# Kernel optimization log

Hardware: AMD Instinct MI355X
Metric: run time of the kernel (lower is better)

Reference implementation:

```python
import jax, jax.numpy as jnp
import numpy as np

B, N, DIM, H = 2, 192, 512, 8
Dh = DIM // H
SCALE = Dh ** -0.5


def setup_inputs() -> dict:
    key = jax.random.key(0)
    ks = jax.random.split(key, 13)
    s = 0.02

    def w(k):
        return jax.random.normal(k, (DIM, DIM), dtype=jnp.float32) * s

    def b(k):
        return jax.random.normal(k, (DIM,), dtype=jnp.float32) * s

    return {
        "queries": jax.random.normal(ks[0], (B, N, DIM), dtype=jnp.float32),
        "keys": jax.random.normal(ks[1], (B, N, DIM), dtype=jnp.float32),
        "values": jax.random.normal(ks[2], (B, N, DIM), dtype=jnp.float32),
        "Wq": w(ks[3]), "bq": b(ks[4]),
        "Wk": w(ks[5]), "bk": b(ks[6]),
        "Wl": w(ks[7]), "bl": b(ks[8]),
        "Wv": w(ks[9]), "bv": b(ks[10]),
        "Wp": w(ks[11]), "bp": b(ks[12]),
    }


def _split_heads(x):
    # [B, N, DIM] -> [B, H, N, Dh]
    return x.reshape(B, N, H, Dh).transpose(0, 2, 1, 3)


def reference(queries, keys, values, Wq, bq, Wk, bk, Wl, bl, Wv, bv, Wp, bp):
    q = _split_heads(queries @ Wq.T + bq) * SCALE
    k = _split_heads(keys @ Wk.T + bk)
    l = _split_heads(keys @ Wl.T + bl)
    v = _split_heads(values @ Wv.T + bv)
    # third-order scores: [B, H, N, N, N]
    attn = jnp.einsum('bhid,bhjd,bhkd->bhijk', q, k, l)
    # softmax over flattened (j, k) axis (valid_lens=None path)
    attn = jax.nn.softmax(attn.reshape(B, H, N, N * N), axis=-1).reshape(B, H, N, N, N)
    # contraction with v_map[b,h,j,k,d] = v[b,h,j,d]*v[b,h,k,d], fused (same math)
    x = jnp.einsum('bhijk,bhjd,bhkd->bhid', attn, v, v)
    x = x.transpose(0, 2, 1, 3).reshape(B, N, DIM)  # merge heads
    return x @ Wp.T + bp
```

## Files before the change

### kernel.cpp

```cpp
#include <hip/hip_runtime.h>

#define B_ 2
#define N_ 192
#define DIM_ 512
#define H_ 8
#define DH_ 64
#define PROJ_ELEMS (B_*H_*N_*DH_)
#define W_ELEMS (DIM_*DIM_)
#define A_ELEMS (B_*N_*DIM_)

typedef __bf16 bf16_t;
typedef __bf16 bf16x4 __attribute__((ext_vector_type(4)));
typedef __bf16 bf16x8 __attribute__((ext_vector_type(8)));
typedef float  f32x16 __attribute__((ext_vector_type(16)));

__device__ __forceinline__ f32x16 mfma32(bf16x8 a, bf16x8 b, f32x16 c) {
    return __builtin_amdgcn_mfma_f32_32x32x16_bf16(a, b, c, 0, 0, 0);
}

union U4 { unsigned int u[4]; bf16x8 v; };

__device__ __forceinline__ unsigned int pack_bf16(float a, float b) {
    unsigned short ua = __builtin_bit_cast(unsigned short, (bf16_t)a);
    unsigned short ub = __builtin_bit_cast(unsigned short, (bf16_t)b);
    return (unsigned int)ua | ((unsigned int)ub << 16);
}
__device__ __forceinline__ float bfbits(unsigned short u) {
    return (float)__builtin_bit_cast(bf16_t, u);
}

struct CArgs {
    const float* src[8];
    bf16_t* dst[8];
    int n[8];
};
__global__ __launch_bounds__(256) void cvt_kernel(CArgs a) {
    const int s = blockIdx.y;
    const int i = (blockIdx.x * 256 + threadIdx.x) * 4;
    if (i < a.n[s]) {
        float4 v = *(const float4*)(a.src[s] + i);
        bf16x4 o;
        o[0] = (bf16_t)v.x; o[1] = (bf16_t)v.y; o[2] = (bf16_t)v.z; o[3] = (bf16_t)v.w;
        *(bf16x4*)(a.dst[s] + i) = o;
    }
}

struct GArgs {
    const bf16_t* A[4];
    const bf16_t* Bm[4];
    const float* bias[4];
    float scale[4];
};

template<int MODE>
__global__ __launch_bounds__(256) void gemm64_kernel(GArgs g, void* outp) {
    const int mat = blockIdx.y;
    const bf16_t* __restrict__ A  = g.A[mat];
    const bf16_t* __restrict__ Bm = g.Bm[mat];

    const int rt = blockIdx.x >> 3, ct = blockIdx.x & 7;
    const int r0 = rt * 64, c0 = ct * 64;
    const int tid = threadIdx.x, wid = tid >> 6, lane = tid & 63;
    const int lo = lane & 31, hi = lane >> 5;
    const int wr = wid >> 1, wc = wid & 1;

    __shared__ __attribute__((aligned(16))) bf16_t As[64 * 64];
    __shared__ __attribute__((aligned(16))) bf16_t Bs[64 * 64];

    f32x16 acc = {};
    for (int k0 = 0; k0 < DIM_; k0 += 64) {
        #pragma unroll
        for (int cch = 0; cch < 2; ++cch) {
            const int d = wid * 2048 + cch * 1024 + lane * 16;
            const int r = d >> 7;
            const int off = (d ^ ((r & 7) << 4)) & 127;
            const char* srcA = (const char*)A + (size_t)(r0 + r) * (DIM_ * 2) + k0 * 2 + off;
            const char* srcB = (const char*)Bm + (size_t)(c0 + r) * (DIM_ * 2) + k0 * 2 + off;
            __builtin_amdgcn_global_load_lds(
                (const __attribute__((address_space(1))) void*)srcA,
                (__attribute__((address_space(3))) void*)((char*)As + wid * 2048 + cch * 1024),
                16, 0, 0);
            __builtin_amdgcn_global_load_lds(
                (const __attribute__((address_space(1))) void*)srcB,
                (__attribute__((address_space(3))) void*)((char*)Bs + wid * 2048 + cch * 1024),
                16, 0, 0);
        }
        __syncthreads();
        const int rowA = wr * 32 + lo, rowB = wc * 32 + lo;
        #pragma unroll
        for (int s = 0; s < 4; ++s) {
            const int ka = (rowA * 128 + s * 32 + hi * 16) ^ ((rowA & 7) << 4);
            const int kb = (rowB * 128 + s * 32 + hi * 16) ^ ((rowB & 7) << 4);
            bf16x8 af = *(const bf16x8*)((const char*)As + ka);
            bf16x8 bf = *(const bf16x8*)((const char*)Bs + kb);
            acc = mfma32(af, bf, acc);
        }
        __syncthreads();
    }

    const int c = c0 + wc * 32 + lo;
    const float bv = g.bias[mat][c];
    if (MODE == 0) {
        const float sc = g.scale[mat];
        const int h = c >> 6, dd = c & 63;
        bf16_t* out = (bf16_t*)outp + (size_t)mat * PROJ_ELEMS;
        #pragma unroll
        for (int r = 0; r < 16; ++r) {
            int row = r0 + wr * 32 + (r & 3) + 8 * (r >> 2) + 4 * hi;
            int bb = (row >= N_) ? 1 : 0;
            int n = row - bb * N_;
            out[(((size_t)(bb * H_ + h)) * N_ + n) * DH_ + dd] = (bf16_t)((acc[r] + bv) * sc);
        }
    } else {
        float* out = (float*)outp;
        #pragma unroll
        for (int r = 0; r < 16; ++r) {
            int row = r0 + wr * 32 + (r & 3) + 8 * (r >> 2) + 4 * hi;
            out[(size_t)row * DIM_ + c] = acc[r] + bv;
        }
    }
}

__global__ __launch_bounds__(256, 3) void attn_kernel(
    const bf16_t* __restrict__ Qg, const bf16_t* __restrict__ Kg,
    const bf16_t* __restrict__ Lg, const bf16_t* __restrict__ Vg,
    bf16_t* __restrict__ Xout)
{
    __shared__ __attribute__((aligned(16))) bf16_t Llds[192 * 72];
    __shared__ __attribute__((aligned(16))) bf16_t VTlds[64 * 200];

    const int bh = blockIdx.y;
    const int tid = threadIdx.x, wid = tid >> 6, lane = tid & 63;
    const int lo = lane & 31, hi = lane >> 5;
    const size_t base = (size_t)bh * (N_ * DH_);

    for (int idx = tid; idx < 1536; idx += 256) {
        int row = idx >> 3, ch = idx & 7;
        *(uint4*)&Llds[row * 72 + ch * 8] = *(const uint4*)(Lg + base + row * 64 + ch * 8);
    }
    for (int idx = tid; idx < 1536; idx += 256) {
        int dc = idx / 192, j = idx - dc * 192;
        bf16x8 v = *(const bf16x8*)(Vg + base + (size_t)j * 64 + dc * 8);
        #pragma unroll
        for (int u = 0; u < 8; ++u)
            VTlds[(dc * 8 + u) * 200 + j] = v[u];
    }
    __syncthreads();

    const int i = blockIdx.x * 4 + wid;
    const bf16_t* qp = Qg + base + (size_t)i * 64;
    bf16x8 qb[4];
    #pragma unroll
    for (int s = 0; s < 4; ++s) qb[s] = *(const bf16x8*)(qp + s * 16 + hi * 8);

    float xacc0 = 0.f, xacc1 = 0.f;
    float Zp[4] = {0.f, 0.f, 0.f, 0.f};

    for (int jb = 0; jb < 6; ++jb) {
        bf16x8 bq[4];
        const bf16_t* kp = Kg + base + (size_t)(jb * 32 + lo) * 64;
        #pragma unroll
        for (int s = 0; s < 4; ++s) {
            bf16x8 kv = *(const bf16x8*)(kp + s * 16 + hi * 8);
            bf16x8 t;
            #pragma unroll
            for (int u = 0; u < 8; ++u) t[u] = (bf16_t)((float)kv[u] * (float)qb[s][u]);
            bq[s] = t;
        }

        f32x16 Tc0 = {}, Tc1 = {};
        #pragma unroll
        for (int kh = 0; kh < 2; ++kh) {
            f32x16 Sc[3];
            #pragma unroll
            for (int kt = 0; kt < 3; ++kt) {
                f32x16 a = {};
                #pragma unroll
                for (int s = 0; s < 4; ++s) {
                    bf16x8 lf = *(const bf16x8*)&Llds[(kh * 96 + kt * 32 + lo) * 72 + s * 16 + hi * 8];
                    a = mfma32(lf, bq[s], a);
                }
                Sc[kt] = a;
            }
            #pragma unroll
            for (int kt = 0; kt < 3; ++kt) {
                float e[16];
                #pragma unroll
                for (int r = 0; r < 16; ++r) {
                    e[r] = __builtin_amdgcn_exp2f(Sc[kt][r]);
                    Zp[r & 3] += e[r];
                }
                #pragma unroll
                for (int sg = 0; sg < 2; ++sg) {
                    unsigned int x0 = pack_bf16(e[8*sg+0], e[8*sg+1]);
                    unsigned int x1 = pack_bf16(e[8*sg+2], e[8*sg+3]);
                    unsigned int y0 = pack_bf16(e[8*sg+4], e[8*sg+5]);
                    unsigned int y1 = pack_bf16(e[8*sg+6], e[8*sg+7]);
                    asm volatile("v_permlane32_swap_b32 %0, %1\n\t"
                                 "v_permlane32_swap_b32 %2, %3"
                                 : "+v"(x0), "+v"(y0), "+v"(x1), "+v"(y1));
                    U4 uf; uf.u[0] = x0; uf.u[1] = x1; uf.u[2] = y0; uf.u[3] = y1;
                    const int tg = kh * 6 + kt * 2 + sg;
                    bf16x8 vf0 = *(const bf16x8*)&VTlds[(0 * 32 + lo) * 200 + tg * 16 + hi * 8];
                    Tc0 = mfma32(uf.v, vf0, Tc0);
                    bf16x8 vf1 = *(const bf16x8*)&VTlds[(1 * 32 + lo) * 200 + tg * 16 + hi * 8];
                    Tc1 = mfma32(uf.v, vf1, Tc1);
                }
            }
        }
        #pragma unroll
        for (int m = 0; m < 4; ++m) {
            const int jj = jb * 32 + m * 8 + 4 * hi;
            ushort4 v0 = *(const ushort4*)&VTlds[(0 * 32 + lo) * 200 + jj];
            ushort4 v1 = *(const ushort4*)&VTlds[(1 * 32 + lo) * 200 + jj];
            xacc0 += Tc0[m*4+0]*bfbits(v0.x) + Tc0[m*4+1]*bfbits(v0.y)
                   + Tc0[m*4+2]*bfbits(v0.z) + Tc0[m*4+3]*bfbits(v0.w);
            xacc1 += Tc1[m*4+0]*bfbits(v1.x) + Tc1[m*4+1]*bfbits(v1.y)
                   + Tc1[m*4+2]*bfbits(v1.z) + Tc1[m*4+3]*bfbits(v1.w);
        }
    }

    float Z = (Zp[0] + Zp[1]) + (Zp[2] + Zp[3]);
    Z += __shfl_xor(Z, 1);
    Z += __shfl_xor(Z, 2);
    Z += __shfl_xor(Z, 4);
    Z += __shfl_xor(Z, 8);
    Z += __shfl_xor(Z, 16);
    Z += __shfl_xor(Z, 32);
    xacc0 += __shfl_xor(xacc0, 32);
    xacc1 += __shfl_xor(xacc1, 32);
    const float invZ = 1.0f / Z;

    if (hi == 0) {
        const int b = bh >> 3, h = bh & 7;
        bf16_t* op = Xout + ((size_t)(b * N_ + i) * DIM_) + h * 64;
        op[lo]      = (bf16_t)(xacc0 * invZ);
        op[32 + lo] = (bf16_t)(xacc1 * invZ);
    }
}

extern "C" void kernel_launch(void* const* d_in, const int* in_sizes, int n_in,
                              void* d_out, int out_size, void* d_ws, size_t ws_size,
                              hipStream_t stream) {
    (void)in_sizes; (void)n_in; (void)out_size; (void)ws_size;
    const float* queries = (const float*)d_in[0];
    const float* keys    = (const float*)d_in[1];
    const float* values  = (const float*)d_in[2];
    const float* Wq = (const float*)d_in[3];
    const float* bq = (const float*)d_in[4];
    const float* Wk = (const float*)d_in[5];
    const float* bk = (const float*)d_in[6];
    const float* Wl = (const float*)d_in[7];
    const float* bl = (const float*)d_in[8];
    const float* Wv = (const float*)d_in[9];
    const float* bv = (const float*)d_in[10];
    const float* Wp = (const float*)d_in[11];
    const float* bp = (const float*)d_in[12];

    bf16_t* Abf = (bf16_t*)d_ws;
    bf16_t* Wbf = Abf + 3 * (size_t)A_ELEMS;
    bf16_t* Pw  = Wbf + 5 * (size_t)W_ELEMS;
    bf16_t* Xw  = Pw  + 4 * (size_t)PROJ_ELEMS;

    CArgs ca;
    ca.src[0] = queries; ca.dst[0] = Abf;               ca.n[0] = A_ELEMS;
    ca.src[1] = keys;    ca.dst[1] = Abf + A_ELEMS;     ca.n[1] = A_ELEMS;
    ca.src[2] = values;  ca.dst[2] = Abf + 2*A_ELEMS;   ca.n[2] = A_ELEMS;
    ca.src[3] = Wq;      ca.dst[3] = Wbf;               ca.n[3] = W_ELEMS;
    ca.src[4] = Wk;      ca.dst[4] = Wbf + W_ELEMS;     ca.n[4] = W_ELEMS;
    ca.src[5] = Wl;      ca.dst[5] = Wbf + 2*W_ELEMS;   ca.n[5] = W_ELEMS;
    ca.src[6] = Wv;      ca.dst[6] = Wbf + 3*W_ELEMS;   ca.n[6] = W_ELEMS;
    ca.src[7] = Wp;      ca.dst[7] = Wbf + 4*W_ELEMS;   ca.n[7] = W_ELEMS;
    cvt_kernel<<<dim3(256, 8), 256, 0, stream>>>(ca);

    GArgs pa;
    pa.A[0] = Abf;             pa.Bm[0] = Wbf;             pa.bias[0] = bq; pa.scale[0] = 0.125f * 1.44269504f;
    pa.A[1] = Abf + A_ELEMS;   pa.Bm[1] = Wbf + W_ELEMS;   pa.bias[1] = bk; pa.scale[1] = 1.0f;
    pa.A[2] = Abf + A_ELEMS;   pa.Bm[2] = Wbf + 2*W_ELEMS; pa.bias[2] = bl; pa.scale[2] = 1.0f;
    pa.A[3] = Abf + 2*A_ELEMS; pa.Bm[3] = Wbf + 3*W_ELEMS; pa.bias[3] = bv; pa.scale[3] = 1.0f;
    gemm64_kernel<0><<<dim3(48, 4), 256, 0, stream>>>(pa, (void*)Pw);

    attn_kernel<<<dim3(48, 16), 256, 0, stream>>>(
        Pw, Pw + PROJ_ELEMS, Pw + 2 * (size_t)PROJ_ELEMS, Pw + 3 * (size_t)PROJ_ELEMS, Xw);

    GArgs fa;
    fa.A[0] = Xw; fa.Bm[0] = Wbf + 4*W_ELEMS; fa.bias[0] = bp; fa.scale[0] = 1.0f;
    fa.A[1] = fa.A[0]; fa.Bm[1] = fa.Bm[0]; fa.bias[1] = fa.bias[0]; fa.scale[1] = 1.0f;
    fa.A[2] = fa.A[0]; fa.Bm[2] = fa.Bm[0]; fa.bias[2] = fa.bias[0]; fa.scale[2] = 1.0f;
    fa.A[3] = fa.A[0]; fa.Bm[3] = fa.Bm[0]; fa.bias[3] = fa.bias[0]; fa.scale[3] = 1.0f;
    gemm64_kernel<1><<<dim3(48, 1), 256, 0, stream>>>(fa, d_out);
}
```

Before: 137.1 us.

## Split k-range across wave pairs and read L from global instead of LDS

Each query row is now handled by two waves, each covering half of the k dimension, and the partial outputs and normalizers are combined through shared memory. The grid doubles to 96x16 blocks. The L tile is no longer staged in LDS; each wave reads its L fragments directly from global memory (cached in L1/L2). Together with the smaller LDS footprint this allows raising launch bounds to 4 blocks per CU, aiming for more parallelism and occupancy. In exchange it repeats global L loads in every jb iteration and adds a block-level reduction with an extra barrier.

```diff
diff --git a/kernel.cpp b/kernel.cpp
--- a/kernel.cpp
+++ b/kernel.cpp
@@ -121,23 +121,21 @@
     }
 }
 
-__global__ __launch_bounds__(256, 3) void attn_kernel(
+__global__ __launch_bounds__(256, 4) void attn_kernel(
     const bf16_t* __restrict__ Qg, const bf16_t* __restrict__ Kg,
     const bf16_t* __restrict__ Lg, const bf16_t* __restrict__ Vg,
     bf16_t* __restrict__ Xout)
 {
-    __shared__ __attribute__((aligned(16))) bf16_t Llds[192 * 72];
     __shared__ __attribute__((aligned(16))) bf16_t VTlds[64 * 200];
-
-    const int bh = blockIdx.y;
+    __shared__ float Xbuf[2][2][64];
+    __shared__ float Zbuf[2][2];
+
     const int tid = threadIdx.x, wid = tid >> 6, lane = tid & 63;
     const int lo = lane & 31, hi = lane >> 5;
+    const int ip = wid >> 1, half = wid & 1;
+    const int bh = blockIdx.y;
     const size_t base = (size_t)bh * (N_ * DH_);
 
-    for (int idx = tid; idx < 1536; idx += 256) {
-        int row = idx >> 3, ch = idx & 7;
-        *(uint4*)&Llds[row * 72 + ch * 8] = *(const uint4*)(Lg + base + row * 64 + ch * 8);
-    }
     for (int idx = tid; idx < 1536; idx += 256) {
         int dc = idx / 192, j = idx - dc * 192;
         bf16x8 v = *(const bf16x8*)(Vg + base + (size_t)j * 64 + dc * 8);
@@ -147,7 +145,7 @@
     }
     __syncthreads();
 
-    const int i = blockIdx.x * 4 + wid;
+    const int i = blockIdx.x * 2 + ip;
     const bf16_t* qp = Qg + base + (size_t)i * 64;
     bf16x8 qb[4];
     #pragma unroll
@@ -168,44 +166,43 @@
             bq[s] = t;
         }
 
+        f32x16 Sc[3];
+        #pragma unroll
+        for (int kt = 0; kt < 3; ++kt) {
+            f32x16 a = {};
+            const bf16_t* lrow = Lg + base + (size_t)(half * 96 + kt * 32 + lo) * 64;
+            #pragma unroll
+            for (int s = 0; s < 4; ++s) {
+                bf16x8 lf = *(const bf16x8*)(lrow + s * 16 + hi * 8);
+                a = mfma32(lf, bq[s], a);
+            }
+            Sc[kt] = a;
+        }
+
         f32x16 Tc0 = {}, Tc1 = {};
         #pragma unroll
-        for (int kh = 0; kh < 2; ++kh) {
-            f32x16 Sc[3];
-            #pragma unroll
-            for (int kt = 0; kt < 3; ++kt) {
-                f32x16 a = {};
-                #pragma unroll
-                for (int s = 0; s < 4; ++s) {
-                    bf16x8 lf = *(const bf16x8*)&Llds[(kh * 96 + kt * 32 + lo) * 72 + s * 16 + hi * 8];
-                    a = mfma32(lf, bq[s], a);
-                }
-                Sc[kt] = a;
+        for (int kt = 0; kt < 3; ++kt) {
+            float e[16];
+            #pragma unroll
+            for (int r = 0; r < 16; ++r) {
+                e[r] = __builtin_amdgcn_exp2f(Sc[kt][r]);
+                Zp[r & 3] += e[r];
             }
             #pragma unroll
-            for (int kt = 0; kt < 3; ++kt) {
-                float e[16];
-                #pragma unroll
-                for (int r = 0; r < 16; ++r) {
-                    e[r] = __builtin_amdgcn_exp2f(Sc[kt][r]);
-                    Zp[r & 3] += e[r];
-                }
-                #pragma unroll
-                for (int sg = 0; sg < 2; ++sg) {
-                    unsigned int x0 = pack_bf16(e[8*sg+0], e[8*sg+1]);
-                    unsigned int x1 = pack_bf16(e[8*sg+2], e[8*sg+3]);
-                    unsigned int y0 = pack_bf16(e[8*sg+4], e[8*sg+5]);
-                    unsigned int y1 = pack_bf16(e[8*sg+6], e[8*sg+7]);
-                    asm volatile("v_permlane32_swap_b32 %0, %1\n\t"
-                                 "v_permlane32_swap_b32 %2, %3"
-                                 : "+v"(x0), "+v"(y0), "+v"(x1), "+v"(y1));
-                    U4 uf; uf.u[0] = x0; uf.u[1] = x1; uf.u[2] = y0; uf.u[3] = y1;
-                    const int tg = kh * 6 + kt * 2 + sg;
-                    bf16x8 vf0 = *(const bf16x8*)&VTlds[(0 * 32 + lo) * 200 + tg * 16 + hi * 8];
-                    Tc0 = mfma32(uf.v, vf0, Tc0);
-                    bf16x8 vf1 = *(const bf16x8*)&VTlds[(1 * 32 + lo) * 200 + tg * 16 + hi * 8];
-                    Tc1 = mfma32(uf.v, vf1, Tc1);
-                }
+            for (int sg = 0; sg < 2; ++sg) {
+                unsigned int x0 = pack_bf16(e[8*sg+0], e[8*sg+1]);
+                unsigned int x1 = pack_bf16(e[8*sg+2], e[8*sg+3]);
+                unsigned int y0 = pack_bf16(e[8*sg+4], e[8*sg+5]);
+                unsigned int y1 = pack_bf16(e[8*sg+6], e[8*sg+7]);
+                asm volatile("v_permlane32_swap_b32 %0, %1\n\t"
+                             "v_permlane32_swap_b32 %2, %3"
+                             : "+v"(x0), "+v"(y0), "+v"(x1), "+v"(y1));
+                U4 uf; uf.u[0] = x0; uf.u[1] = x1; uf.u[2] = y0; uf.u[3] = y1;
+                const int tg = half * 6 + kt * 2 + sg;
+                bf16x8 vf0 = *(const bf16x8*)&VTlds[(0 * 32 + lo) * 200 + tg * 16 + hi * 8];
+                Tc0 = mfma32(uf.v, vf0, Tc0);
+                bf16x8 vf1 = *(const bf16x8*)&VTlds[(1 * 32 + lo) * 200 + tg * 16 + hi * 8];
+                Tc1 = mfma32(uf.v, vf1, Tc1);
             }
         }
         #pragma unroll
@@ -220,6 +217,8 @@
         }
     }
 
+    xacc0 += __shfl_xor(xacc0, 32);
+    xacc1 += __shfl_xor(xacc1, 32);
     float Z = (Zp[0] + Zp[1]) + (Zp[2] + Zp[3]);
     Z += __shfl_xor(Z, 1);
     Z += __shfl_xor(Z, 2);
@@ -227,15 +226,21 @@
     Z += __shfl_xor(Z, 8);
     Z += __shfl_xor(Z, 16);
     Z += __shfl_xor(Z, 32);
-    xacc0 += __shfl_xor(xacc0, 32);
-    xacc1 += __shfl_xor(xacc1, 32);
-    const float invZ = 1.0f / Z;
 
     if (hi == 0) {
+        Xbuf[ip][half][lo]      = xacc0;
+        Xbuf[ip][half][32 + lo] = xacc1;
+    }
+    if (lane == 0) Zbuf[ip][half] = Z;
+    __syncthreads();
+
+    if (tid < 128) {
+        const int ipo = tid >> 6, l = tid & 63;
+        const int io = blockIdx.x * 2 + ipo;
+        const float v = Xbuf[ipo][0][l] + Xbuf[ipo][1][l];
+        const float invZ = 1.0f / (Zbuf[ipo][0] + Zbuf[ipo][1]);
         const int b = bh >> 3, h = bh & 7;
-        bf16_t* op = Xout + ((size_t)(b * N_ + i) * DIM_) + h * 64;
-        op[lo]      = (bf16_t)(xacc0 * invZ);
-        op[32 + lo] = (bf16_t)(xacc1 * invZ);
+        Xout[((size_t)(b * N_ + io) * DIM_) + h * 64 + l] = (bf16_t)(v * invZ);
     }
 }
 
@@ -280,7 +285,7 @@
     pa.A[3] = Abf + 2*A_ELEMS; pa.Bm[3] = Wbf + 3*W_ELEMS; pa.bias[3] = bv; pa.scale[3] = 1.0f;
     gemm64_kernel<0><<<dim3(48, 4), 256, 0, stream>>>(pa, (void*)Pw);
 
-    attn_kernel<<<dim3(48, 16), 256, 0, stream>>>(
+    attn_kernel<<<dim3(96, 16), 256, 0, stream>>>(
         Pw, Pw + PROJ_ELEMS, Pw + 2 * (size_t)PROJ_ELEMS, Pw + 3 * (size_t)PROJ_ELEMS, Xw);
 
     GArgs fa;
```

Measured after the change: 194.7 us. 1.42x slower.
